# Kernel tuning notes

Measured on AMD Instinct MI355X. Metric: run time of the kernel, lower is better.

Reference implementation:

```python
import jax, jax.numpy as jnp
from jax import lax
import numpy as np

B, T, C = 4, 2048, 1024
H = 4                      # num_heads
D = C // H                 # head_dim
EPS_N = 1e-6               # normalizer eps in scan
EPS_GN = 1e-5              # GroupNorm eps (torch default)


def setup_inputs() -> dict:
    key = jax.random.key(0)
    ks = jax.random.split(key, 8)
    s = 0.02
    return {
        "x": jax.random.normal(ks[0], (B, T, C), jnp.float32),
        "conv_w": jax.random.normal(ks[1], (C, 1, 4), jnp.float32) * s,
        "conv_b": jax.random.normal(ks[2], (C,), jnp.float32) * s,
        "wx_w": jax.random.normal(ks[3], (4 * C, C), jnp.float32) * s,
        "wx_b": jax.random.normal(ks[4], (4 * C,), jnp.float32) * s,
        "gn_w": jnp.ones((C,), jnp.float32),
        "gn_b": jnp.zeros((C,), jnp.float32),
        "out_w": jax.random.normal(ks[5], (C, C), jnp.float32) * s,
        "out_b": jax.random.normal(ks[6], (C,), jnp.float32) * s,
    }


def _slstm_scan(i_g, f_g, z_g, o_g):
    # all inputs (B,T,H,D); scan over time
    def step(carry, g):
        c, n, m = carry
        i_t, f_t, z_t, o_t = g
        m_t = jnp.maximum(f_t + m, i_t)
        i_p = jnp.exp(i_t - m_t)
        f_p = jnp.exp(f_t + m - m_t)
        c_t = f_p * c + i_p * z_t
        n_t = f_p * n + i_p
        h_t = jax.nn.sigmoid(o_t) * (c_t / (n_t + EPS_N))
        return (c_t, n_t, m_t), h_t

    tfirst = lambda a: jnp.transpose(a, (1, 0, 2, 3))  # (T,B,H,D)
    init = (jnp.zeros((B, H, D), i_g.dtype),
            jnp.ones((B, H, D), i_g.dtype),
            jnp.zeros((B, H, D), i_g.dtype))
    _, h_seq = lax.scan(step, init, (tfirst(i_g), tfirst(f_g), tfirst(z_g), tfirst(o_g)))
    return jnp.transpose(h_seq, (1, 0, 2, 3))  # (B,T,H,D)


def reference(x, conv_w, conv_b, wx_w, wx_b, gn_w, gn_b, out_w, out_b):
    # causal depthwise conv (torch pad=3 both sides, sliced to first T == left pad 3)
    xc = jnp.transpose(x, (0, 2, 1))  # (B,C,T)
    xc = lax.conv_general_dilated(
        xc, conv_w, window_strides=(1,), padding=[(3, 0)],
        dimension_numbers=("NCH", "OIH", "NCH"), feature_group_count=C)
    xc = jax.nn.silu(xc + conv_b[None, :, None])
    xc = jnp.transpose(xc, (0, 2, 1))  # (B,T,C)

    gates = jnp.einsum("btc,gc->btg", xc, wx_w) + wx_b  # (B,T,4C)
    gates = gates.reshape(B, T, 4, H, D)
    i_g, f_g, z_g, o_g = (gates[:, :, k] for k in range(4))
    z_g = jnp.tanh(z_g)

    h = _slstm_scan(i_g, f_g, z_g, o_g).reshape(B, T, C)

    # GroupNorm(H groups) over (B,C,T): normalize per (batch, group) over (D, T)
    hg = h.reshape(B, T, H, D)
    mean = hg.mean(axis=(1, 3), keepdims=True)
    var = hg.var(axis=(1, 3), keepdims=True)
    hn = ((hg - mean) / jnp.sqrt(var + EPS_GN)).reshape(B, T, C)
    hn = hn * gn_w + gn_b

    out = jnp.einsum("btc,oc->bto", hn, out_w) + out_b
    return out + x  # dropout is identity at inference
```

## Files before the change

kernel.cpp:

```cpp
#include <hip/hip_runtime.h>

#define B_ 4
#define T_ 2048
#define C_ 1024
#define H_ 4
#define D_ 256
#define M_ (B_*T_)
#define N1_ (4*C_)
#define K_ C_
#define LANES_ (B_*C_)
#define CHUNK_ 32
#define NCHUNK_ (T_/CHUNK_)

typedef unsigned short u16;
typedef unsigned int u32;
typedef __bf16 bf16x8 __attribute__((ext_vector_type(8)));
typedef float f32x4 __attribute__((ext_vector_type(4)));
typedef float vf4 __attribute__((ext_vector_type(4)));
typedef unsigned short u16x4 __attribute__((ext_vector_type(4)));
typedef unsigned short u16x8 __attribute__((ext_vector_type(8)));

__device__ __forceinline__ u16 f2bf(float f) {
  union { float f; u32 u; } v; v.f = f;
  u32 u = v.u;
  u32 r = (u + 0x7FFFu + ((u >> 16) & 1u)) >> 16;
  return (u16)r;
}
__device__ __forceinline__ float b2f(u16 h) {
  union { u32 u; float f; } v; v.u = ((u32)h) << 16;
  return v.f;
}

#define NCAST_ ((N1_*K_ + C_*C_) / 2048)

__global__ void prep_kernel(const float* __restrict__ wx_w, const float* __restrict__ out_w,
                            u16* __restrict__ w1p, u16* __restrict__ w2,
                            const float* __restrict__ x, const float* __restrict__ cw,
                            const float* __restrict__ cb, u16* __restrict__ xc,
                            float* __restrict__ stats) {
  if (blockIdx.x < NCAST_) {
    int i8 = (blockIdx.x * 256 + threadIdx.x) * 8;
    u16x8 o;
    if (i8 < N1_ * K_) {
      int n = i8 >> 10, k8 = i8 & 1023;
      const float* src = wx_w + (size_t)(((n & 3) << 10) | (n >> 2)) * K_ + k8;
      vf4 a = *(const vf4*)src;
      vf4 b = *(const vf4*)(src + 4);
#pragma unroll
      for (int j = 0; j < 4; ++j) { o[j] = f2bf(a[j]); o[j + 4] = f2bf(b[j]); }
      *(u16x8*)(w1p + i8) = o;
    } else {
      int j8 = i8 - N1_ * K_;
      vf4 a = *(const vf4*)(out_w + j8);
      vf4 b = *(const vf4*)(out_w + j8 + 4);
#pragma unroll
      for (int j = 0; j < 4; ++j) { o[j] = f2bf(a[j]); o[j + 4] = f2bf(b[j]); }
      *(u16x8*)(w2 + j8) = o;
    }
    return;
  }
  if (blockIdx.x == NCAST_ && threadIdx.x < 32) stats[threadIdx.x] = 0.f;
  int i4 = ((blockIdx.x - NCAST_) * 256 + threadIdx.x) * 4;
  int c = i4 & (C_ - 1);
  int t = (i4 >> 10) & (T_ - 1);
  vf4 acc = *(const vf4*)(cb + c);
  vf4 w0 = *(const vf4*)(cw + (size_t)c * 4);
  vf4 w1 = *(const vf4*)(cw + (size_t)(c + 1) * 4);
  vf4 w2v = *(const vf4*)(cw + (size_t)(c + 2) * 4);
  vf4 w3 = *(const vf4*)(cw + (size_t)(c + 3) * 4);
#pragma unroll
  for (int k = 0; k < 4; ++k) {
    if (t - 3 + k >= 0) {
      vf4 xv = *(const vf4*)(x + (size_t)i4 + (size_t)(k - 3) * C_);
      acc[0] = fmaf(w0[k], xv[0], acc[0]);
      acc[1] = fmaf(w1[k], xv[1], acc[1]);
      acc[2] = fmaf(w2v[k], xv[2], acc[2]);
      acc[3] = fmaf(w3[k], xv[3], acc[3]);
    }
  }
  u16x4 o;
#pragma unroll
  for (int j = 0; j < 4; ++j) {
    float s = acc[j] / (1.f + __expf(-acc[j]));
    o[j] = f2bf(s);
  }
  *(u16x4*)(xc + i4) = o;
}

template <int EPI>
__global__ __launch_bounds__(256, 3)
void gemm_bt(const u16* __restrict__ A, const u16* __restrict__ Bw,
             const float* __restrict__ bias, const float* __restrict__ resid,
             u16* __restrict__ obf, float* __restrict__ of32,
             f32x4* __restrict__ sSum, int M, int N, int K)
{
  __shared__ __align__(16) u16 smem[128 * 136];
  u16* a_s = smem;
  u16* b_s = smem + 128 * 64;

  const int tid  = threadIdx.x;
  const int lane = tid & 63;
  const int l15  = lane & 15;
  const int q    = lane >> 4;
  const int wave = tid >> 6;
  const int wm   = (wave >> 1) * 64;
  const int wn   = (wave & 1) * 64;
  const int bm   = blockIdx.y * 128;
  const int bn   = blockIdx.x * 128;

  const int srow   = wave * 8 + (lane >> 3);
  const int schunk = lane & 7;

  float bias4[4];
#pragma unroll
  for (int sn = 0; sn < 4; ++sn) {
    int gcol = bn + wn + sn * 16 + l15;
    bias4[sn] = (EPI == 0) ? bias[((gcol & 3) << 10) | (gcol >> 2)] : bias[gcol];
  }
  const bool zlane = (EPI == 0) && ((l15 & 3) == 2);

  f32x4 acc[4][4];
#pragma unroll
  for (int i = 0; i < 4; ++i)
#pragma unroll
    for (int j = 0; j < 4; ++j) acc[i][j] = (f32x4){0.f, 0.f, 0.f, 0.f};

  for (int k0 = 0; k0 < K; k0 += 64) {
#pragma unroll
    for (int i = 0; i < 4; ++i) {
      int r = i * 32 + srow;
      int lc = schunk ^ (r & 7);
      const u16* ga = A  + (size_t)(bm + r) * K + k0 + lc * 8;
      const u16* gb = Bw + (size_t)(bn + r) * K + k0 + lc * 8;
      __builtin_amdgcn_global_load_lds(
          (const __attribute__((address_space(1))) u32*)ga,
          (__attribute__((address_space(3))) u32*)&a_s[(i * 32 + wave * 8) * 64],
          16, 0, 0);
      __builtin_amdgcn_global_load_lds(
          (const __attribute__((address_space(1))) u32*)gb,
          (__attribute__((address_space(3))) u32*)&b_s[(i * 32 + wave * 8) * 64],
          16, 0, 0);
    }
    __syncthreads();
#pragma unroll
    for (int kk = 0; kk < 64; kk += 32) {
      const int kc = kk >> 3;
      bf16x8 af[4], bfr[4];
#pragma unroll
      for (int s = 0; s < 4; ++s) {
        int ra = wm + s * 16 + l15;
        int ph = (kc + q) ^ (ra & 7);
        af[s] = *(const bf16x8*)&a_s[ra * 64 + ph * 8];
      }
#pragma unroll
      for (int s = 0; s < 4; ++s) {
        int rb = wn + s * 16 + l15;
        int ph = (kc + q) ^ (rb & 7);
        bfr[s] = *(const bf16x8*)&b_s[rb * 64 + ph * 8];
      }
#pragma unroll
      for (int sm = 0; sm < 4; ++sm)
#pragma unroll
        for (int sn = 0; sn < 4; ++sn)
          acc[sm][sn] = __builtin_amdgcn_mfma_f32_16x16x32_bf16(af[sm], bfr[sn], acc[sm][sn], 0, 0, 0);
    }
    __syncthreads();
  }

  if (EPI == 0) {
    __shared__ __align__(16) f32x4 seg[256];
#pragma unroll
    for (int smi = 0; smi < 4; ++smi) {
#pragma unroll
      for (int r = 0; r < 4; ++r) {
        int lrow = wm + smi * 16 + q * 4 + r;
#pragma unroll
        for (int sni = 0; sni < 4; ++sni) {
          int lcol = wn + sni * 16 + l15;
          float v = acc[smi][sni][r] + bias4[sni];
          if (zlane) {
            float e = __expf(2.f * v);
            v = (e - 1.f) / (e + 1.f);
          }
          smem[lrow * 136 + lcol] = f2bf(v);
        }
      }
    }
    __syncthreads();
#pragma unroll
    for (int it = 0; it < 8; ++it) {
      int flat = it * 256 + tid;
      int row = flat >> 4;
      int ch  = flat & 15;
      u16x8 vv = *(const u16x8*)&smem[row * 136 + ch * 8];
      *(u16x8*)(obf + (size_t)(bm + row) * N + bn + ch * 8) = vv;
    }
    {
      int unit = tid & 127;
      int half = tid >> 7;
      int ch = unit & 31, ck = unit >> 5;
      const u16* sp = smem + (ck * 32 + half * 16) * 136 + ch * 4;
      float F = 0.f, Mx = -1e30f, aBc = 0.f, aBn = 0.f;
#pragma unroll
      for (int t = 0; t < 16; ++t) {
        u16x4 gv = *(const u16x4*)(sp + t * 136);
        float i_t = b2f(gv[0]), f_t = b2f(gv[1]), z_t = b2f(gv[2]);
        float Mf = Mx + f_t;
        float Mn = fmaxf(Mf, i_t);
        float ea = __expf(Mf - Mn), eb = __expf(i_t - Mn);
        aBc = ea * aBc + eb * z_t;
        aBn = ea * aBn + eb;
        F += f_t; Mx = Mn;
      }
      seg[tid] = (f32x4){F, Mx, aBc, aBn};
    }
    __syncthreads();
    if (tid < 128) {
      f32x4 s0 = seg[tid], s1 = seg[tid + 128];
      float F = s0[0] + s1[0];
      float Mx = fmaxf(s0[1] + s1[0], s1[1]);
      float e0 = __expf(s0[1] + s1[0] - Mx), e1 = __expf(s1[1] - Mx);
      float aBc = e0 * s0[2] + e1 * s1[2];
      float aBn = e0 * s0[3] + e1 * s1[3];
      int ch = tid & 31, ck = tid >> 5;
      int b = bm >> 11;
      int s = ((bm & 2047) >> 5) + ck;
      int cg = (bn >> 2) + ch;
      sSum[(size_t)s * LANES_ + b * C_ + cg] = (f32x4){F, Mx, aBc, aBn};
    }
  } else {
    float* fs = (float*)smem;
#pragma unroll
    for (int h = 0; h < 2; ++h) {
      __syncthreads();
#pragma unroll
      for (int smi2 = 0; smi2 < 2; ++smi2) {
        int smi = 2 * h + smi2;
#pragma unroll
        for (int r = 0; r < 4; ++r) {
          int slot = (wm >> 1) + smi2 * 16 + q * 4 + r;
#pragma unroll
          for (int sni = 0; sni < 4; ++sni) {
            int lcol = wn + sni * 16 + l15;
            fs[slot * 132 + lcol] = acc[smi][sni][r] + bias4[sni];
          }
        }
      }
      __syncthreads();
#pragma unroll
      for (int it = 0; it < 8; ++it) {
        int flat = it * 256 + tid;
        int slot = flat >> 5;
        int c4 = (flat & 31) * 4;
        int absrow = bm + ((slot & 32) << 1) + (h << 5) + (slot & 31);
        vf4 v = *(const vf4*)&fs[slot * 132 + c4];
        vf4 rv = *(const vf4*)(resid + (size_t)absrow * N + bn + c4);
        v[0] += rv[0]; v[1] += rv[1]; v[2] += rv[2]; v[3] += rv[3];
        *(vf4*)(of32 + (size_t)absrow * N + bn + c4) = v;
      }
    }
  }
}

__global__ void scan_local(const u16* __restrict__ gates, const f32x4* __restrict__ sSum,
                           u16* __restrict__ h, float* __restrict__ stats) {
  const int thr = threadIdx.x;
  const int tid = blockIdx.x * 256 + thr;
  const int lp = tid & 2047;
  const int s = tid >> 11;
  const int b = lp >> 9;
  const int c2 = (lp & 511) * 2;
  const int base = b * C_ + c2;

  float cc0 = 0.f, nn0 = 1.f, mm0 = 0.f;
  float cc1 = 0.f, nn1 = 1.f, mm1 = 0.f;
  for (int j = 0; j < s; ++j) {
    f32x4 S0 = sSum[(size_t)j * LANES_ + base];
    f32x4 S1 = sSum[(size_t)j * LANES_ + base + 1];
    {
      float mf = mm0 + S0[0];
      float mn = fmaxf(mf, S0[1]);
      float a = __expf(mf - mn), bc = __expf(S0[1] - mn);
      cc0 = a * cc0 + bc * S0[2];
      nn0 = a * nn0 + bc * S0[3];
      mm0 = mn;
    }
    {
      float mf = mm1 + S1[0];
      float mn = fmaxf(mf, S1[1]);
      float a = __expf(mf - mn), bc = __expf(S1[1] - mn);
      cc1 = a * cc1 + bc * S1[2];
      nn1 = a * nn1 + bc * S1[3];
      mm1 = mn;
    }
  }

  const u16* g = gates + ((size_t)(b * T_ + s * CHUNK_) * C_ + c2) * 4;
  u16* hp = h + (size_t)(b * T_ + s * CHUNK_) * C_ + c2;
  float ls = 0.f, lq = 0.f;
#pragma unroll 4
  for (int t = 0; t < CHUNK_; ++t) {
    u16x8 gv = *(const u16x8*)(g + (size_t)t * C_ * 4);
    float h0, h1;
    {
      float i_t = b2f(gv[0]), f_t = b2f(gv[1]), z_t = b2f(gv[2]), o_t = b2f(gv[3]);
      float m_new = fmaxf(f_t + mm0, i_t);
      float i_p = __expf(i_t - m_new);
      float f_p = __expf(f_t + mm0 - m_new);
      cc0 = f_p * cc0 + i_p * z_t;
      nn0 = f_p * nn0 + i_p;
      mm0 = m_new;
      float sig_o = 1.f / (1.f + __expf(-o_t));
      h0 = sig_o * (cc0 / (nn0 + 1e-6f));
    }
    {
      float i_t = b2f(gv[4]), f_t = b2f(gv[5]), z_t = b2f(gv[6]), o_t = b2f(gv[7]);
      float m_new = fmaxf(f_t + mm1, i_t);
      float i_p = __expf(i_t - m_new);
      float f_p = __expf(f_t + mm1 - m_new);
      cc1 = f_p * cc1 + i_p * z_t;
      nn1 = f_p * nn1 + i_p;
      mm1 = m_new;
      float sig_o = 1.f / (1.f + __expf(-o_t));
      h1 = sig_o * (cc1 / (nn1 + 1e-6f));
    }
    u16 hb0 = f2bf(h0), hb1 = f2bf(h1);
    float v0 = b2f(hb0), v1 = b2f(hb1);
    ls += v0 + v1; lq += v0 * v0 + v1 * v1;
    *(u32*)(hp + (size_t)t * C_) = (u32)hb0 | ((u32)hb1 << 16);
  }
  __shared__ float rs[256], rq[256];
  rs[thr] = ls; rq[thr] = lq;
  __syncthreads();
  for (int off = 64; off > 0; off >>= 1) {
    if ((thr & 127) < off) { rs[thr] += rs[thr + off]; rq[thr] += rq[thr + off]; }
    __syncthreads();
  }
  if ((thr & 127) == 0) {
    int grp = b * 4 + (c2 >> 8);
    atomicAdd(&stats[grp * 2 + 0], rs[thr]);
    atomicAdd(&stats[grp * 2 + 1], rq[thr]);
  }
}

__global__ void norm_kernel(const u16* __restrict__ h, const float* __restrict__ stats,
                            const float* __restrict__ gn_w, const float* __restrict__ gn_b,
                            u16* __restrict__ hn) {
  int i8 = (blockIdx.x * 256 + threadIdx.x) * 8;
  int c = i8 & (C_ - 1);
  int b = i8 >> 21;
  int grp = b * 4 + (c >> 8);
  const float inv_n = 1.f / (float)(T_ * D_);
  float mean = stats[grp * 2 + 0] * inv_n;
  float var  = stats[grp * 2 + 1] * inv_n - mean * mean;
  float rstd = rsqrtf(var + 1e-5f);
  u16x8 hv = *(const u16x8*)(h + i8);
  vf4 w0 = *(const vf4*)(gn_w + c), w1 = *(const vf4*)(gn_w + c + 4);
  vf4 b0 = *(const vf4*)(gn_b + c), b1 = *(const vf4*)(gn_b + c + 4);
  u16x8 o;
#pragma unroll
  for (int j = 0; j < 4; ++j) {
    o[j]     = f2bf((b2f(hv[j])     - mean) * rstd * w0[j] + b0[j]);
    o[j + 4] = f2bf((b2f(hv[j + 4]) - mean) * rstd * w1[j] + b1[j]);
  }
  *(u16x8*)(hn + i8) = o;
}

extern "C" void kernel_launch(void* const* d_in, const int* in_sizes, int n_in,
                              void* d_out, int out_size, void* d_ws, size_t ws_size,
                              hipStream_t stream) {
  const float* x      = (const float*)d_in[0];
  const float* conv_w = (const float*)d_in[1];
  const float* conv_b = (const float*)d_in[2];
  const float* wx_w   = (const float*)d_in[3];
  const float* wx_b   = (const float*)d_in[4];
  const float* gn_w   = (const float*)d_in[5];
  const float* gn_b   = (const float*)d_in[6];
  const float* out_w  = (const float*)d_in[7];
  const float* out_b  = (const float*)d_in[8];
  float* out = (float*)d_out;

  char* p = (char*)d_ws;
  u16* xc    = (u16*)p; p += (size_t)M_ * K_ * 2;
  u16* w1    = (u16*)p; p += (size_t)N1_ * K_ * 2;
  u16* w2    = (u16*)p; p += (size_t)C_ * C_ * 2;
  u16* gts   = (u16*)p; p += (size_t)M_ * N1_ * 2;
  u16* hb    = (u16*)p; p += (size_t)M_ * C_ * 2;
  u16* hn    = (u16*)p; p += (size_t)M_ * C_ * 2;
  float* stats = (float*)p; p += 256;
  const int nsum = LANES_ * NCHUNK_;
  f32x4* sSum = (f32x4*)p; p += (size_t)nsum * 16;

  prep_kernel<<<NCAST_ + (M_ * C_) / 1024, 256, 0, stream>>>(
      wx_w, out_w, w1, w2, x, conv_w, conv_b, xc, stats);

  gemm_bt<0><<<dim3(N1_ / 128, M_ / 128), 256, 0, stream>>>(
      xc, w1, wx_b, nullptr, gts, nullptr, sSum, M_, N1_, K_);

  scan_local<<<512, 256, 0, stream>>>(gts, sSum, hb, stats);

  norm_kernel<<<(M_ * C_) / 2048, 256, 0, stream>>>(hb, stats, gn_w, gn_b, hn);

  gemm_bt<1><<<dim3(C_ / 128, M_ / 128), 256, 0, stream>>>(
      hn, w2, out_b, x, nullptr, out, nullptr, M_, C_, K_);
}
```

Measured before the change: 277.5 us.

## Fuse GroupNorm into scan kernel via grid-wide atomic barrier

Merges the scan and GroupNorm kernels: each thread keeps its chunk of h in registers, block partial sums are accumulated atomically, then all blocks spin on a global counter before applying normalization and writing hn directly. This removes the intermediate h buffer round trip through memory and one kernel launch. It relies on all 512 blocks being co-resident and adds register pressure from the 32-entry per-thread buffer, with a risk of deadlock or reduced occupancy.

```diff
diff --git a/kernel.cpp b/kernel.cpp
--- a/kernel.cpp
+++ b/kernel.cpp
@@ -37,7 +37,7 @@
                             u16* __restrict__ w1p, u16* __restrict__ w2,
                             const float* __restrict__ x, const float* __restrict__ cw,
                             const float* __restrict__ cb, u16* __restrict__ xc,
-                            float* __restrict__ stats) {
+                            float* __restrict__ stats, int* __restrict__ flags) {
   if (blockIdx.x < NCAST_) {
     int i8 = (blockIdx.x * 256 + threadIdx.x) * 8;
     u16x8 o;
@@ -59,7 +59,10 @@
     }
     return;
   }
-  if (blockIdx.x == NCAST_ && threadIdx.x < 32) stats[threadIdx.x] = 0.f;
+  if (blockIdx.x == NCAST_) {
+    if (threadIdx.x < 32) stats[threadIdx.x] = 0.f;
+    else if (threadIdx.x < 48) flags[threadIdx.x - 32] = 0;
+  }
   int i4 = ((blockIdx.x - NCAST_) * 256 + threadIdx.x) * 4;
   int c = i4 & (C_ - 1);
   int t = (i4 >> 10) & (T_ - 1);
@@ -262,8 +265,10 @@
   }
 }
 
-__global__ void scan_local(const u16* __restrict__ gates, const f32x4* __restrict__ sSum,
-                           u16* __restrict__ h, float* __restrict__ stats) {
+__global__ void scan_norm(const u16* __restrict__ gates, const f32x4* __restrict__ sSum,
+                          u16* __restrict__ hn, const float* __restrict__ gn_w,
+                          const float* __restrict__ gn_b, float* __restrict__ stats,
+                          int* __restrict__ flags) {
   const int thr = threadIdx.x;
   const int tid = blockIdx.x * 256 + thr;
   const int lp = tid & 2047;
@@ -296,8 +301,8 @@
   }
 
   const u16* g = gates + ((size_t)(b * T_ + s * CHUNK_) * C_ + c2) * 4;
-  u16* hp = h + (size_t)(b * T_ + s * CHUNK_) * C_ + c2;
   float ls = 0.f, lq = 0.f;
+  u32 hreg[CHUNK_];
 #pragma unroll 4
   for (int t = 0; t < CHUNK_; ++t) {
     u16x8 gv = *(const u16x8*)(g + (size_t)t * C_ * 4);
@@ -327,7 +332,7 @@
     u16 hb0 = f2bf(h0), hb1 = f2bf(h1);
     float v0 = b2f(hb0), v1 = b2f(hb1);
     ls += v0 + v1; lq += v0 * v0 + v1 * v1;
-    *(u32*)(hp + (size_t)t * C_) = (u32)hb0 | ((u32)hb1 << 16);
+    hreg[t] = (u32)hb0 | ((u32)hb1 << 16);
   }
   __shared__ float rs[256], rq[256];
   rs[thr] = ls; rq[thr] = lq;
@@ -336,34 +341,36 @@
     if ((thr & 127) < off) { rs[thr] += rs[thr + off]; rq[thr] += rq[thr + off]; }
     __syncthreads();
   }
+  const int grp = b * 4 + (c2 >> 8);
   if ((thr & 127) == 0) {
-    int grp = b * 4 + (c2 >> 8);
     atomicAdd(&stats[grp * 2 + 0], rs[thr]);
     atomicAdd(&stats[grp * 2 + 1], rq[thr]);
   }
-}
-
-__global__ void norm_kernel(const u16* __restrict__ h, const float* __restrict__ stats,
-                            const float* __restrict__ gn_w, const float* __restrict__ gn_b,
-                            u16* __restrict__ hn) {
-  int i8 = (blockIdx.x * 256 + threadIdx.x) * 8;
-  int c = i8 & (C_ - 1);
-  int b = i8 >> 21;
-  int grp = b * 4 + (c >> 8);
+  __syncthreads();
+  if (thr == 0) {
+    __hip_atomic_fetch_add(&flags[0], 1, __ATOMIC_RELEASE, __HIP_MEMORY_SCOPE_AGENT);
+    while (__hip_atomic_load(&flags[0], __ATOMIC_RELAXED, __HIP_MEMORY_SCOPE_AGENT) < 512)
+      __builtin_amdgcn_s_sleep(8);
+  }
+  __syncthreads();
+
   const float inv_n = 1.f / (float)(T_ * D_);
-  float mean = stats[grp * 2 + 0] * inv_n;
-  float var  = stats[grp * 2 + 1] * inv_n - mean * mean;
+  float sum = __hip_atomic_load(&stats[grp * 2 + 0], __ATOMIC_RELAXED, __HIP_MEMORY_SCOPE_AGENT);
+  float sumsq = __hip_atomic_load(&stats[grp * 2 + 1], __ATOMIC_RELAXED, __HIP_MEMORY_SCOPE_AGENT);
+  float mean = sum * inv_n;
+  float var  = sumsq * inv_n - mean * mean;
   float rstd = rsqrtf(var + 1e-5f);
-  u16x8 hv = *(const u16x8*)(h + i8);
-  vf4 w0 = *(const vf4*)(gn_w + c), w1 = *(const vf4*)(gn_w + c + 4);
-  vf4 b0 = *(const vf4*)(gn_b + c), b1 = *(const vf4*)(gn_b + c + 4);
-  u16x8 o;
-#pragma unroll
-  for (int j = 0; j < 4; ++j) {
-    o[j]     = f2bf((b2f(hv[j])     - mean) * rstd * w0[j] + b0[j]);
-    o[j + 4] = f2bf((b2f(hv[j + 4]) - mean) * rstd * w1[j] + b1[j]);
-  }
-  *(u16x8*)(hn + i8) = o;
+  float w_0 = gn_w[c2], w_1 = gn_w[c2 + 1];
+  float bb0 = gn_b[c2], bb1 = gn_b[c2 + 1];
+  u16* hp = hn + (size_t)(b * T_ + s * CHUNK_) * C_ + c2;
+#pragma unroll 4
+  for (int t = 0; t < CHUNK_; ++t) {
+    u32 hv = hreg[t];
+    float v0 = b2f((u16)hv), v1 = b2f((u16)(hv >> 16));
+    u16 o0 = f2bf((v0 - mean) * rstd * w_0 + bb0);
+    u16 o1 = f2bf((v1 - mean) * rstd * w_1 + bb1);
+    *(u32*)(hp + (size_t)t * C_) = (u32)o0 | ((u32)o1 << 16);
+  }
 }
 
 extern "C" void kernel_launch(void* const* d_in, const int* in_sizes, int n_in,
@@ -385,21 +392,19 @@
   u16* w1    = (u16*)p; p += (size_t)N1_ * K_ * 2;
   u16* w2    = (u16*)p; p += (size_t)C_ * C_ * 2;
   u16* gts   = (u16*)p; p += (size_t)M_ * N1_ * 2;
-  u16* hb    = (u16*)p; p += (size_t)M_ * C_ * 2;
   u16* hn    = (u16*)p; p += (size_t)M_ * C_ * 2;
-  float* stats = (float*)p; p += 256;
+  float* stats = (float*)p; p += 128;
+  int* flags = (int*)p; p += 128;
   const int nsum = LANES_ * NCHUNK_;
   f32x4* sSum = (f32x4*)p; p += (size_t)nsum * 16;
 
   prep_kernel<<<NCAST_ + (M_ * C_) / 1024, 256, 0, stream>>>(
-      wx_w, out_w, w1, w2, x, conv_w, conv_b, xc, stats);
+      wx_w, out_w, w1, w2, x, conv_w, conv_b, xc, stats, flags);
 
   gemm_bt<0><<<dim3(N1_ / 128, M_ / 128), 256, 0, stream>>>(
       xc, w1, wx_b, nullptr, gts, nullptr, sSum, M_, N1_, K_);
 
-  scan_local<<<512, 256, 0, stream>>>(gts, sSum, hb, stats);
-
-  norm_kernel<<<(M_ * C_) / 2048, 256, 0, stream>>>(hb, stats, gn_w, gn_b, hn);
+  scan_norm<<<512, 256, 0, stream>>>(gts, sSum, hn, gn_w, gn_b, stats, flags);
 
   gemm_bt<1><<<dim3(C_ / 128, M_ / 128), 256, 0, stream>>>(
       hn, w2, out_b, x, nullptr, out, nullptr, M_, C_, K_);
```

Result: slower. 325.4 us (+17.3%).
